# Kernel optimization log

Hardware: AMD Instinct MI355X
Metric: run time of the kernel (lower is better)

The kernel has to match this reference:

```python
import jax, jax.numpy as jnp
import numpy as np

NUM_LAYERS = 2
SEQ_LEN = 128
HIDDEN = 512
OUTPUT = 512
BATCH = 512


def setup_inputs() -> dict:
    key = jax.random.key(0)
    ks = jax.random.split(key, 12)
    k = 1.0 / np.sqrt(HIDDEN)
    u = lambda kk, shape: jax.random.uniform(kk, shape, jnp.float32, -k, k)
    return {
        "x": jax.random.normal(ks[0], (BATCH, HIDDEN), jnp.float32),
        # stacked per-layer LSTM params, PyTorch gate order (i, f, g, o)
        "W_ih": u(ks[1], (NUM_LAYERS, 4 * HIDDEN, HIDDEN)),
        "W_hh": u(ks[2], (NUM_LAYERS, 4 * HIDDEN, HIDDEN)),
        "b_ih": u(ks[3], (NUM_LAYERS, 4 * HIDDEN)),
        "b_hh": u(ks[4], (NUM_LAYERS, 4 * HIDDEN)),
        # 3-layer MLP head
        "fc1_w": u(ks[5], (HIDDEN, HIDDEN)),
        "fc1_b": u(ks[6], (HIDDEN,)),
        "fc2_w": u(ks[7], (HIDDEN, HIDDEN)),
        "fc2_b": u(ks[8], (HIDDEN,)),
        "fc3_w": u(ks[9], (OUTPUT, HIDDEN)),
        "fc3_b": u(ks[10], (OUTPUT,)),
    }


def reference(x, W_ih, W_hh, b_ih, b_hh, fc1_w, fc1_b, fc2_w, fc2_b, fc3_w, fc3_b):
    B, H = x.shape
    L = W_ih.shape[0]
    h0 = jnp.zeros((L, B, H), x.dtype)
    c0 = jnp.zeros((L, B, H), x.dtype)

    def step(carry, _):
        h, c, inp = carry  # h,c: [L,B,H]; inp: [B,H]
        x_l = inp
        hs, cs = [], []
        for l in range(L):  # small fixed layer loop
            gates = x_l @ W_ih[l].T + b_ih[l] + h[l] @ W_hh[l].T + b_hh[l]
            i, f, g, o = jnp.split(gates, 4, axis=-1)
            c_new = jax.nn.sigmoid(f) * c[l] + jax.nn.sigmoid(i) * jnp.tanh(g)
            h_new = jax.nn.sigmoid(o) * jnp.tanh(c_new)
            hs.append(h_new)
            cs.append(c_new)
            x_l = h_new
        h = jnp.stack(hs)
        c = jnp.stack(cs)
        h_sum = h.sum(0)  # torch.sum(h_t, 0) over layers
        return (h, c, h_sum), h_sum  # next input is summed hidden

    _, outs = jax.lax.scan(step, (h0, c0, x), None, length=SEQ_LEN)
    out = jnp.transpose(outs, (1, 0, 2))  # [B, seq_len, H]
    out = jax.nn.relu(out @ fc1_w.T + fc1_b)
    out = jax.nn.relu(out @ fc2_w.T + fc2_b)
    out = out @ fc3_w.T + fc3_b  # [B, seq_len, output_size]
    return out
```

## Files before the change

### kernel.cpp

```cpp
#include <hip/hip_runtime.h>
#include <cstdint>
#include <cstddef>


using u16 = unsigned short;
typedef __attribute__((ext_vector_type(8))) _Float16 f16x8;
typedef __attribute__((ext_vector_type(4))) float f32x4;

__device__ __forceinline__ u16 f2h(float f) {
    union { _Float16 h; u16 u; } v; v.h = (_Float16)f; return v.u;
}
__device__ __forceinline__ float h2f(u16 u) {
    union { u16 u; _Float16 h; } v; v.u = u; return (float)v.h;
}
__device__ __forceinline__ float tanh_fast(float v) {
    float a = fabsf(v);
    float t = __expf(-2.f * a);
    float r = (1.f - t) / (1.f + t);
    return copysignf(r, v);
}
__device__ __forceinline__ float sigmoid_fast(float v) {
    return 1.f / (1.f + __expf(-v));
}

__device__ __forceinline__ void gl_lds16(const u16* g, char* l) {
    __builtin_amdgcn_global_load_lds((const __attribute__((address_space(1))) char*)(const char*)g,
                                     (__attribute__((address_space(3))) char*)l, 16, 0, 0);
}

__device__ __forceinline__ f16x8 lds_read_sw(const u16* tile, int row, int cu) {
    int unit = (row << 3) | (cu ^ (row & 7));
    return *(const f16x8*)&tile[unit << 3];
}

__global__ __launch_bounds__(256) void prepack(
    const float* __restrict__ W_ih, const float* __restrict__ W_hh,
    const float* __restrict__ b_ih, const float* __restrict__ b_hh,
    const float* __restrict__ fc1w, const float* __restrict__ fc2w, const float* __restrict__ fc3w,
    u16* __restrict__ Bpack, float* __restrict__ bsumv, u16* __restrict__ fcw)
{
    int stride = gridDim.x * blockDim.x;
    int tid0 = blockIdx.x * blockDim.x + threadIdx.x;
    for (int idx = tid0; idx < 2 * 2048 * 1024; idx += stride) {
        int l = idx >> 21;
        int rem = idx & ((1 << 21) - 1);
        int np = rem >> 10;
        int k = rem & 1023;
        int n = (np & 3) * 512 + (np >> 2);
        float v = (k < 512) ? W_ih[((size_t)l * 2048 + n) * 512 + k]
                            : W_hh[((size_t)l * 2048 + n) * 512 + (k - 512)];
        Bpack[idx] = f2h(v);
    }
    for (int idx = tid0; idx < 2 * 2048; idx += stride) {
        int l = idx >> 11;
        int np = idx & 2047;
        int n = (np & 3) * 512 + (np >> 2);
        bsumv[idx] = b_ih[l * 2048 + n] + b_hh[l * 2048 + n];
    }
    for (int idx = tid0; idx < 3 * 512 * 512; idx += stride) {
        const float* w = idx < 262144 ? fc1w : (idx < 524288 ? fc2w : fc3w);
        fcw[idx] = f2h(w[idx & 262143]);
    }
}

__global__ __launch_bounds__(256) void initbufs(
    const float* __restrict__ x, u16* __restrict__ A0_0, u16* __restrict__ A1_0,
    float* __restrict__ c0, float* __restrict__ c1, float* __restrict__ gb0)
{
    int stride = gridDim.x * blockDim.x;
    int tid0 = blockIdx.x * blockDim.x + threadIdx.x;
    for (int idx = tid0; idx < 512 * 512; idx += stride) {
        int row = idx >> 9, col = idx & 511;
        size_t b = (size_t)row * 1024;
        A0_0[b + col] = f2h(x[idx]);
        A1_0[b + 512 + col] = 0;
        c0[idx] = 0.f;
        c1[idx] = 0.f;
    }
    for (int idx = tid0; idx < 1048576; idx += stride) gb0[idx] = 0.f;
}

template <int IS_L1>
__global__ __launch_bounds__(256) void lstm_phase(
    const u16* __restrict__ Ax, const u16* __restrict__ Ah, int hoffH,
    const u16* __restrict__ Wc, const u16* __restrict__ Wp,
    const float* __restrict__ gbufR, float* __restrict__ gbufW,
    const float* __restrict__ bsumv, float* __restrict__ cbuf,
    u16* __restrict__ hdst, const u16* __restrict__ h0src,
    u16* __restrict__ hsumdst, u16* __restrict__ seqdst)
{
    __shared__ char smem[49152];

    const int id = blockIdx.x;
    const bool isPartial = id >= 256;
    const int rid = id & 255;
    const int xcd = rid & 7, slot = rid >> 3;
    const int nb = xcd * 4 + (slot & 3);
    const int rg = slot >> 2;
    const int n0 = nb * 64;
    const int row0 = rg * 64;
    const int tile = rg * 32 + nb;

    const u16* Abase = isPartial ? Ah : Ax;
    const int xoff = isPartial ? hoffH : 0;
    const u16* Wbase = isPartial ? Wp : Wc;

    const int tid = threadIdx.x;
    const int lane = tid & 63, wid = tid >> 6;
    const int wm = (wid >> 1) * 32, wn = (wid & 1) * 32;
    const int fm = lane & 15, q = lane >> 4;

    const int s0 = wid * 128 + lane, s1 = s0 + 64;
    const int r0s = s0 >> 3, c0s = ((s0 & 7) ^ (r0s & 7)) << 3;
    const int r1s = s1 >> 3, c1s = ((s1 & 7) ^ (r1s & 7)) << 3;
    const size_t aO0 = (size_t)(row0 + r0s) * 1024 + xoff + c0s;
    const size_t aO1 = (size_t)(row0 + r1s) * 1024 + xoff + c1s;
    const size_t bO0 = (size_t)(n0 + r0s) * 1024 + c0s;
    const size_t bO1 = (size_t)(n0 + r1s) * 1024 + c1s;
    const int d0 = wid * 2048, d1 = d0 + 1024;

    f32x4 acc[2][2];
    acc[0][0] = (f32x4)0.f; acc[0][1] = (f32x4)0.f;
    acc[1][0] = (f32x4)0.f; acc[1][1] = (f32x4)0.f;

    auto stage = [&](char* buf, int k0) {
        gl_lds16(Abase + aO0 + k0, buf + d0);
        gl_lds16(Abase + aO1 + k0, buf + d1);
        gl_lds16(Wbase + bO0 + k0, buf + 8192 + d0);
        gl_lds16(Wbase + bO1 + k0, buf + 8192 + d1);
    };

    char* p0 = smem;
    char* p1 = smem + 16384;
    char* p2 = smem + 32768;

    stage(p0, 0);
    stage(p1, 64);

    for (int c = 0; c < 8; ++c) {
        if (c < 7) asm volatile("s_waitcnt vmcnt(4)" ::: "memory");
        else       asm volatile("s_waitcnt vmcnt(0)" ::: "memory");
        __builtin_amdgcn_s_barrier();
        if (c < 6) stage(p2, (c + 2) * 64);
        __builtin_amdgcn_sched_barrier(0);

        const u16* sA = (const u16*)p0;
        const u16* sB = (const u16*)(p0 + 8192);

#pragma unroll
        for (int kf = 0; kf < 2; ++kf) {
            const int cu = kf * 4 + q;
            f16x8 b0 = lds_read_sw(sB, wn + fm, cu);
            f16x8 b1 = lds_read_sw(sB, wn + 16 + fm, cu);
            f16x8 a0 = lds_read_sw(sA, wm + fm, cu);
            f16x8 a1 = lds_read_sw(sA, wm + 16 + fm, cu);
            acc[0][0] = __builtin_amdgcn_mfma_f32_16x16x32_f16(b0, a0, acc[0][0], 0, 0, 0);
            acc[0][1] = __builtin_amdgcn_mfma_f32_16x16x32_f16(b0, a1, acc[0][1], 0, 0, 0);
            acc[1][0] = __builtin_amdgcn_mfma_f32_16x16x32_f16(b1, a0, acc[1][0], 0, 0, 0);
            acc[1][1] = __builtin_amdgcn_mfma_f32_16x16x32_f16(b1, a1, acc[1][1], 0, 0, 0);
        }

        char* t = p0; p0 = p1; p1 = p2; p2 = t;
    }

    if (isPartial) {
        float* dst = gbufW + (size_t)tile * 4096 + wid * 1024 + lane * 4;
        *(f32x4*)(dst +   0) = acc[0][0];
        *(f32x4*)(dst + 256) = acc[0][1];
        *(f32x4*)(dst + 512) = acc[1][0];
        *(f32x4*)(dst + 768) = acc[1][1];
        return;
    }

    {
        const float* src = gbufR + (size_t)tile * 4096 + wid * 1024 + lane * 4;
        acc[0][0] += *(const f32x4*)(src +   0);
        acc[0][1] += *(const f32x4*)(src + 256);
        acc[1][0] += *(const f32x4*)(src + 512);
        acc[1][1] += *(const f32x4*)(src + 768);
    }

    __syncthreads();
    u16* hb = (u16*)smem;

#pragma unroll
    for (int i = 0; i < 2; ++i)
#pragma unroll
    for (int jj = 0; jj < 2; ++jj) {
        const int hcl = ((wn + i * 16) >> 2) + q;
        const int bl  = wm + jj * 16 + fm;
        const float4 b4 = *(const float4*)&bsumv[n0 + wn + i * 16 + q * 4];
        float gi = acc[i][jj][0] + b4.x;
        float gf = acc[i][jj][1] + b4.y;
        float gg = acc[i][jj][2] + b4.z;
        float go = acc[i][jj][3] + b4.w;
        const int cidx = ((n0 >> 2) + hcl) * 512 + (row0 + bl);
        float c_old = cbuf[cidx];
        float is = sigmoid_fast(gi);
        float fs = sigmoid_fast(gf);
        float os = sigmoid_fast(go);
        float gt = tanh_fast(gg);
        float cn = fs * c_old + is * gt;
        float hn = os * tanh_fast(cn);
        cbuf[cidx] = cn;
        hb[bl * 16 + hcl] = f2h(hn);
    }
    __syncthreads();

    {
        const int bl = tid >> 2;
        const int hc4 = (tid & 3) * 4;
        const int grow = row0 + bl;
        const int gh = (n0 >> 2) + hc4;
        ushort4 h4 = *(const ushort4*)&hb[bl * 16 + hc4];
        const size_t ab = (size_t)grow * 1024;
        if (!IS_L1) {
            *(ushort4*)&hdst[ab + gh] = h4;
        } else {
            *(ushort4*)&hdst[ab + 512 + gh] = h4;
            ushort4 h0v = *(const ushort4*)&h0src[ab + gh];
            ushort4 s4;
            s4.x = f2h(h2f(h0v.x) + h2f(h4.x));
            s4.y = f2h(h2f(h0v.y) + h2f(h4.y));
            s4.z = f2h(h2f(h0v.z) + h2f(h4.z));
            s4.w = f2h(h2f(h0v.w) + h2f(h4.w));
            *(ushort4*)&hsumdst[ab + gh] = s4;
            *(ushort4*)&seqdst[(size_t)grow * 512 + gh] = s4;
        }
    }
}

template <int RELU, int FINAL>
__global__ __launch_bounds__(256) void mlp_gemm(
    const u16* __restrict__ A, const u16* __restrict__ Bw, const float* __restrict__ bias,
    u16* __restrict__ yh, float* __restrict__ yf32)
{
    __shared__ char smem[36864];
    u16* sA = (u16*)smem;
    u16* sB = (u16*)(smem + 9216);

    const int tid = threadIdx.x;
    const int lane = tid & 63, wid = tid >> 6;
    const int row0 = blockIdx.y * 64;
    const int n0 = blockIdx.x * 128;
    const int wn = wid * 32;
    const int fm = lane & 15;
    const int fkbase = (lane >> 4) * 8;

    f32x4 acc[4][2];
#pragma unroll
    for (int m = 0; m < 4; ++m) { acc[m][0] = (f32x4)0.f; acc[m][1] = (f32x4)0.f; }

    for (int kk = 0; kk < 8; ++kk) {
        const int k0 = kk * 64;
        __syncthreads();
#pragma unroll
        for (int r = 0; r < 2; ++r) {
            int c = tid + r * 256;
            int row = c >> 3, cc = (c & 7) * 8;
            *(f16x8*)&sA[row * 72 + cc] = *(const f16x8*)&A[(size_t)(row0 + row) * 512 + k0 + cc];
        }
#pragma unroll
        for (int r = 0; r < 4; ++r) {
            int c = tid + r * 256;
            int row = c >> 3, cc = (c & 7) * 8;
            *(f16x8*)&sB[row * 72 + cc] = *(const f16x8*)&Bw[(size_t)(n0 + row) * 512 + k0 + cc];
        }
        __syncthreads();
#pragma unroll
        for (int kf = 0; kf < 2; ++kf) {
            const int kb = kf * 32 + fkbase;
            f16x8 b0 = *(const f16x8*)&sB[(wn + fm) * 72 + kb];
            f16x8 b1 = *(const f16x8*)&sB[(wn + 16 + fm) * 72 + kb];
#pragma unroll
            for (int m = 0; m < 4; ++m) {
                f16x8 ah = *(const f16x8*)&sA[(m * 16 + fm) * 72 + kb];
                acc[m][0] = __builtin_amdgcn_mfma_f32_16x16x32_f16(ah, b0, acc[m][0], 0, 0, 0);
                acc[m][1] = __builtin_amdgcn_mfma_f32_16x16x32_f16(ah, b1, acc[m][1], 0, 0, 0);
            }
        }
    }

    __syncthreads();
    float* sG = (float*)smem;
#pragma unroll
    for (int m = 0; m < 4; ++m)
#pragma unroll
        for (int n = 0; n < 2; ++n)
#pragma unroll
            for (int r = 0; r < 4; ++r) {
                int row = m * 16 + (lane >> 4) * 4 + r;
                int col = wn + n * 16 + fm;
                sG[row * 132 + col] = acc[m][n][r];
            }
    __syncthreads();

    const int row = tid >> 2;
    const int cg = (tid & 3) * 32;
    const size_t r = (size_t)row0 + row;
#pragma unroll
    for (int c = cg; c < cg + 32; c += 4) {
        float4 g = *(const float4*)&sG[row * 132 + c];
        float4 b = *(const float4*)&bias[n0 + c];
        float v0 = g.x + b.x, v1 = g.y + b.y, v2 = g.z + b.z, v3 = g.w + b.w;
        if (RELU) {
            v0 = fmaxf(v0, 0.f); v1 = fmaxf(v1, 0.f); v2 = fmaxf(v2, 0.f); v3 = fmaxf(v3, 0.f);
        }
        if (!FINAL) {
            ushort4 p;
            p.x = f2h(v0); p.y = f2h(v1); p.z = f2h(v2); p.w = f2h(v3);
            *(ushort4*)&yh[r * 512 + n0 + c] = p;
        } else {
            int tt = (int)(r >> 9), bb = (int)(r & 511);
            float4 o; o.x = v0; o.y = v1; o.z = v2; o.w = v3;
            *(float4*)&yf32[((size_t)bb * 128 + tt) * 512 + n0 + c] = o;
        }
    }
}

extern "C" void kernel_launch(void* const* d_in, const int* in_sizes, int n_in,
                              void* d_out, int out_size, void* d_ws, size_t ws_size,
                              hipStream_t stream) {
    const float* x    = (const float*)d_in[0];
    const float* W_ih = (const float*)d_in[1];
    const float* W_hh = (const float*)d_in[2];
    const float* b_ih = (const float*)d_in[3];
    const float* b_hh = (const float*)d_in[4];
    const float* fc1w = (const float*)d_in[5];
    const float* fc1b = (const float*)d_in[6];
    const float* fc2w = (const float*)d_in[7];
    const float* fc2b = (const float*)d_in[8];
    const float* fc3w = (const float*)d_in[9];
    const float* fc3b = (const float*)d_in[10];

    char* ws = (char*)d_ws;
    u16* Bpack = (u16*)(ws);
    u16* fcw   = (u16*)(ws + 8388608);
    float* bsum = (float*)(ws + 9961472);
    u16* A0[2] = { (u16*)(ws + 9977856),  (u16*)(ws + 11026432) };
    u16* A1[2] = { (u16*)(ws + 12075008), (u16*)(ws + 13123584) };
    float* c0 = (float*)(ws + 14172160);
    float* c1 = (float*)(ws + 15220736);
    u16* seqb = (u16*)(ws + 20463616);
    float* gb[2] = { (float*)(ws + 87572480), (float*)(ws + 87572480 + 4194304) };
    u16* y1   = (u16*)(ws + 87572480);
    float* out = (float*)d_out;

    prepack<<<dim3(512), dim3(256), 0, stream>>>(W_ih, W_hh, b_ih, b_hh, fc1w, fc2w, fc3w,
                                                 Bpack, bsum, fcw);
    initbufs<<<dim3(512), dim3(256), 0, stream>>>(x, A0[0], A1[0], c0, c1, gb[0]);

    const int LSTR = 2048 * 1024;
    for (int s = 0; s < 256; ++s) {
        int t = s >> 1, layer = s & 1, cur = t & 1, nxt = cur ^ 1;
        float* gR = gb[s & 1];
        float* gW = gb[(s + 1) & 1];
        if (!layer) {
            lstm_phase<0><<<dim3(512), dim3(256), 0, stream>>>(
                A0[cur], A1[cur], 512, Bpack, Bpack + LSTR + 512,
                gR, gW, bsum, c0,
                A1[cur], nullptr, nullptr, nullptr);
        } else {
            lstm_phase<1><<<dim3(512), dim3(256), 0, stream>>>(
                A1[cur], A1[cur], 0, Bpack + LSTR, Bpack + 512,
                gR, gW, bsum + 2048, c1,
                A1[nxt], A1[cur], A0[nxt], seqb + (size_t)t * 262144);
        }
    }

    mlp_gemm<1, 0><<<dim3(4, 1024), dim3(256), 0, stream>>>(seqb, fcw, fc1b, y1, nullptr);
    mlp_gemm<1, 0><<<dim3(4, 1024), dim3(256), 0, stream>>>(y1, fcw + 512 * 512, fc2b, seqb, nullptr);
    mlp_gemm<0, 1><<<dim3(4, 1024), dim3(256), 0, stream>>>(seqb, fcw + 2 * 512 * 512, fc3b, nullptr, out);
}
```

Measured before the change: 1.957 ms.

## Enlarge MLP GEMM tile to 128x128 with double-buffered direct-to-LDS loads

The MLP head GEMM moves from 64x128 tiles to 128x128 tiles. Each wave now computes a 64x64 sub-tile, which raises MFMA reuse per LDS read. Global-to-LDS direct loads with an XOR-swizzled layout are double-buffered so the next K slice loads while the current one computes. The epilogue is staged in two halves through shared memory, and the grid is halved. The kernel now uses 64KB of LDS, which may limit occupancy.

```diff
diff --git a/kernel.cpp b/kernel.cpp
--- a/kernel.cpp
+++ b/kernel.cpp
@@ -235,86 +235,111 @@
     const u16* __restrict__ A, const u16* __restrict__ Bw, const float* __restrict__ bias,
     u16* __restrict__ yh, float* __restrict__ yf32)
 {
-    __shared__ char smem[36864];
-    u16* sA = (u16*)smem;
-    u16* sB = (u16*)(smem + 9216);
+    __shared__ char smem[65536];
 
     const int tid = threadIdx.x;
     const int lane = tid & 63, wid = tid >> 6;
-    const int row0 = blockIdx.y * 64;
+    const int row0 = blockIdx.y * 128;
     const int n0 = blockIdx.x * 128;
-    const int wn = wid * 32;
-    const int fm = lane & 15;
-    const int fkbase = (lane >> 4) * 8;
-
-    f32x4 acc[4][2];
-#pragma unroll
-    for (int m = 0; m < 4; ++m) { acc[m][0] = (f32x4)0.f; acc[m][1] = (f32x4)0.f; }
-
-    for (int kk = 0; kk < 8; ++kk) {
-        const int k0 = kk * 64;
+    const int wm = (wid >> 1) * 64, wn = (wid & 1) * 64;
+    const int fm = lane & 15, q = lane >> 4;
+
+    int rS[4], cS[4];
+#pragma unroll
+    for (int i = 0; i < 4; ++i) {
+        int s = wid * 256 + i * 64 + lane;
+        rS[i] = s >> 3; cS[i] = ((s & 7) ^ (rS[i] & 7)) << 3;
+    }
+    size_t aO[4], bO[4];
+#pragma unroll
+    for (int i = 0; i < 4; ++i) {
+        aO[i] = (size_t)(row0 + rS[i]) * 512 + cS[i];
+        bO[i] = (size_t)(n0 + rS[i]) * 512 + cS[i];
+    }
+    const int dst0 = wid * 4096;
+
+    f32x4 acc[4][4];
+#pragma unroll
+    for (int m = 0; m < 4; ++m)
+#pragma unroll
+        for (int n = 0; n < 4; ++n) acc[m][n] = (f32x4)0.f;
+
+    auto stage = [&](char* buf, int k0) {
+#pragma unroll
+        for (int i = 0; i < 4; ++i) gl_lds16(A + aO[i] + k0, buf + dst0 + i * 1024);
+#pragma unroll
+        for (int i = 0; i < 4; ++i) gl_lds16(Bw + bO[i] + k0, buf + 16384 + dst0 + i * 1024);
+    };
+
+    char* pc = smem;
+    char* pn = smem + 32768;
+
+    stage(pc, 0);
+    __syncthreads();
+
+    for (int c = 0; c < 8; ++c) {
+        if (c + 1 < 8) stage(pn, (c + 1) * 64);
+
+        const u16* sA = (const u16*)pc;
+        const u16* sB = (const u16*)(pc + 16384);
+
+#pragma unroll
+        for (int kf = 0; kf < 2; ++kf) {
+            const int cu = kf * 4 + q;
+            f16x8 a[4], b[4];
+#pragma unroll
+            for (int m = 0; m < 4; ++m) a[m] = lds_read_sw(sA, wm + m * 16 + fm, cu);
+#pragma unroll
+            for (int n = 0; n < 4; ++n) b[n] = lds_read_sw(sB, wn + n * 16 + fm, cu);
+#pragma unroll
+            for (int m = 0; m < 4; ++m)
+#pragma unroll
+                for (int n = 0; n < 4; ++n)
+                    acc[m][n] = __builtin_amdgcn_mfma_f32_16x16x32_f16(a[m], b[n], acc[m][n], 0, 0, 0);
+        }
+
         __syncthreads();
-#pragma unroll
-        for (int r = 0; r < 2; ++r) {
-            int c = tid + r * 256;
-            int row = c >> 3, cc = (c & 7) * 8;
-            *(f16x8*)&sA[row * 72 + cc] = *(const f16x8*)&A[(size_t)(row0 + row) * 512 + k0 + cc];
-        }
-#pragma unroll
-        for (int r = 0; r < 4; ++r) {
-            int c = tid + r * 256;
-            int row = c >> 3, cc = (c & 7) * 8;
-            *(f16x8*)&sB[row * 72 + cc] = *(const f16x8*)&Bw[(size_t)(n0 + row) * 512 + k0 + cc];
+        char* t = pc; pc = pn; pn = t;
+    }
+
+    float* sG = (float*)smem;
+#pragma unroll
+    for (int h = 0; h < 2; ++h) {
+        if ((wid >> 1) == h) {
+#pragma unroll
+            for (int m = 0; m < 4; ++m)
+#pragma unroll
+                for (int n = 0; n < 4; ++n)
+#pragma unroll
+                    for (int r = 0; r < 4; ++r) {
+                        int row = m * 16 + q * 4 + r;
+                        int col = wn + n * 16 + fm;
+                        sG[row * 132 + col] = acc[m][n][r];
+                    }
         }
         __syncthreads();
-#pragma unroll
-        for (int kf = 0; kf < 2; ++kf) {
-            const int kb = kf * 32 + fkbase;
-            f16x8 b0 = *(const f16x8*)&sB[(wn + fm) * 72 + kb];
-            f16x8 b1 = *(const f16x8*)&sB[(wn + 16 + fm) * 72 + kb];
-#pragma unroll
-            for (int m = 0; m < 4; ++m) {
-                f16x8 ah = *(const f16x8*)&sA[(m * 16 + fm) * 72 + kb];
-                acc[m][0] = __builtin_amdgcn_mfma_f32_16x16x32_f16(ah, b0, acc[m][0], 0, 0, 0);
-                acc[m][1] = __builtin_amdgcn_mfma_f32_16x16x32_f16(ah, b1, acc[m][1], 0, 0, 0);
+        const int rloc = tid >> 2;
+        const int cg = (tid & 3) * 32;
+        const size_t r = (size_t)row0 + h * 64 + rloc;
+#pragma unroll
+        for (int cc = cg; cc < cg + 32; cc += 4) {
+            float4 g = *(const float4*)&sG[rloc * 132 + cc];
+            float4 b = *(const float4*)&bias[n0 + cc];
+            float v0 = g.x + b.x, v1 = g.y + b.y, v2 = g.z + b.z, v3 = g.w + b.w;
+            if (RELU) {
+                v0 = fmaxf(v0, 0.f); v1 = fmaxf(v1, 0.f); v2 = fmaxf(v2, 0.f); v3 = fmaxf(v3, 0.f);
             }
-        }
-    }
-
-    __syncthreads();
-    float* sG = (float*)smem;
-#pragma unroll
-    for (int m = 0; m < 4; ++m)
-#pragma unroll
-        for (int n = 0; n < 2; ++n)
-#pragma unroll
-            for (int r = 0; r < 4; ++r) {
-                int row = m * 16 + (lane >> 4) * 4 + r;
-                int col = wn + n * 16 + fm;
-                sG[row * 132 + col] = acc[m][n][r];
+            if (!FINAL) {
+                ushort4 p;
+                p.x = f2h(v0); p.y = f2h(v1); p.z = f2h(v2); p.w = f2h(v3);
+                *(ushort4*)&yh[r * 512 + n0 + cc] = p;
+            } else {
+                int tt = (int)(r >> 9), bb = (int)(r & 511);
+                float4 o; o.x = v0; o.y = v1; o.z = v2; o.w = v3;
+                *(float4*)&yf32[((size_t)bb * 128 + tt) * 512 + n0 + cc] = o;
             }
-    __syncthreads();
-
-    const int row = tid >> 2;
-    const int cg = (tid & 3) * 32;
-    const size_t r = (size_t)row0 + row;
-#pragma unroll
-    for (int c = cg; c < cg + 32; c += 4) {
-        float4 g = *(const float4*)&sG[row * 132 + c];
-        float4 b = *(const float4*)&bias[n0 + c];
-        float v0 = g.x + b.x, v1 = g.y + b.y, v2 = g.z + b.z, v3 = g.w + b.w;
-        if (RELU) {
-            v0 = fmaxf(v0, 0.f); v1 = fmaxf(v1, 0.f); v2 = fmaxf(v2, 0.f); v3 = fmaxf(v3, 0.f);
-        }
-        if (!FINAL) {
-            ushort4 p;
-            p.x = f2h(v0); p.y = f2h(v1); p.z = f2h(v2); p.w = f2h(v3);
-            *(ushort4*)&yh[r * 512 + n0 + c] = p;
-        } else {
-            int tt = (int)(r >> 9), bb = (int)(r & 511);
-            float4 o; o.x = v0; o.y = v1; o.z = v2; o.w = v3;
-            *(float4*)&yf32[((size_t)bb * 128 + tt) * 512 + n0 + c] = o;
-        }
+        }
+        __syncthreads();
     }
 }
 
@@ -368,7 +393,7 @@
         }
     }
 
-    mlp_gemm<1, 0><<<dim3(4, 1024), dim3(256), 0, stream>>>(seqb, fcw, fc1b, y1, nullptr);
-    mlp_gemm<1, 0><<<dim3(4, 1024), dim3(256), 0, stream>>>(y1, fcw + 512 * 512, fc2b, seqb, nullptr);
-    mlp_gemm<0, 1><<<dim3(4, 1024), dim3(256), 0, stream>>>(seqb, fcw + 2 * 512 * 512, fc3b, nullptr, out);
-}
+    mlp_gemm<1, 0><<<dim3(4, 512), dim3(256), 0, stream>>>(seqb, fcw, fc1b, y1, nullptr);
+    mlp_gemm<1, 0><<<dim3(4, 512), dim3(256), 0, stream>>>(y1, fcw + 512 * 512, fc2b, seqb, nullptr);
+    mlp_gemm<0, 1><<<dim3(4, 512), dim3(256), 0, stream>>>(seqb, fcw + 2 * 512 * 512, fc3b, nullptr, out);
+}
```

Measured after the change: 1.958 ms. About the same (+0.1%).
